# Kernel optimization log

Hardware: AMD Instinct MI355X
Metric: run time of the kernel (lower is better)

Reference implementation:

```python
import jax, jax.numpy as jnp
import numpy as np

E = 800_000      # number of edges
D = 256          # d_model_edge
N = 50_000       # number of atoms/nodes


def setup_inputs() -> dict:
    key = jax.random.key(0)
    k1, k2, k3, k4, k5 = jax.random.split(key, 5)
    forces = jax.random.normal(k1, (E, D), dtype=jnp.float32)
    V_st = jax.random.normal(k2, (E, 3), dtype=jnp.float32)
    # MLP([D, D, 1]): Linear(D,D) + act + Linear(D,1). Scaled init for stability.
    W1 = jax.random.normal(k3, (D, D), dtype=jnp.float32) * (1.0 / np.sqrt(D))
    b1 = jnp.zeros((D,), dtype=jnp.float32)
    W2 = jax.random.normal(k4, (D, 1), dtype=jnp.float32) * (1.0 / np.sqrt(D))
    b2 = jnp.zeros((1,), dtype=jnp.float32)
    idx_t = jax.random.randint(k5, (E,), 0, N, dtype=jnp.int64 if jax.config.jax_enable_x64 else jnp.int32)
    return {
        "forces": forces,
        "V_st": V_st,
        "W1": W1,
        "b1": b1,
        "W2": W2,
        "b2": b2,
        "idx_t": idx_t,
        "n_atoms": N,
    }


def reference(forces, V_st, W1, b1, W2, b2, idx_t, n_atoms):
    # out_mlp: Linear(D,D) -> SiLU -> Linear(D,1)
    h = jax.nn.silu(forces @ W1 + b1)          # [E, D]
    s = h @ W2 + b2                            # [E, 1] per-edge scalar
    ev = s * V_st                              # [E, 3] scaled direction vectors
    # scatter-sum over target node indices (reduction='sum')
    out = jax.ops.segment_sum(ev, idx_t, num_segments=n_atoms)  # [N, 3]
    return out
```

## Files before the change

kernel.cpp:

```cpp
#include <hip/hip_runtime.h>
#include <hip/hip_bf16.h>

typedef __attribute__((ext_vector_type(8))) short short8;
typedef __attribute__((ext_vector_type(4))) float floatx4;
typedef unsigned short u16;

#define D 256
#define BM 128
#define NT 512

__device__ __forceinline__ short f2bf(float f) {
    return __builtin_bit_cast(short, __float2bfloat16(f));
}

__global__ void w1f_kernel(const float* __restrict__ W1, u16* __restrict__ W1F) {
    const int k = blockIdx.x, n = threadIdx.x;
    const int k0t = k >> 5, g = (k >> 3) & 3, j = k & 7;
    const int nt = n >> 4, l15 = n & 15;
    W1F[(long)((((k0t << 4) + nt) << 6) + (g << 4) + l15) * 8 + j] = (u16)f2bf(W1[k * D + n]);
}

__launch_bounds__(NT, 4)
__global__ void head_kernel(const float* __restrict__ forces,
                            const float* __restrict__ V_st,
                            const u16*   __restrict__ W1F,
                            const float* __restrict__ b1,
                            const float* __restrict__ W2,
                            const float* __restrict__ b2,
                            const int*   __restrict__ idx_t,
                            float* __restrict__ out,
                            int E) {
    __shared__ u16 Abuf[BM * D];
    __shared__ float s_red[4][BM];

    const int tid  = threadIdx.x;
    const int lane = tid & 63;
    const int w    = tid >> 6;
    const int wm   = w >> 2;
    const int wn   = w & 3;
    const int l15  = lane & 15;
    const int g    = lane >> 4;

    const long blk_row = (long)blockIdx.x * BM;

#pragma unroll
    for (int it = 0; it < 8; ++it) {
        int c   = it * NT + tid;
        int row = c >> 5;
        int kc  = (c & 31) * 8;
        long grow = blk_row + row;
        if (grow > (long)E - 1) grow = (long)E - 1;
        const float* src = forces + grow * D + kc;
        floatx4 f0 = *(const floatx4*)(src);
        floatx4 f1 = *(const floatx4*)(src + 4);
        short8 a;
#pragma unroll
        for (int jj = 0; jj < 4; ++jj) { a[jj] = f2bf(f0[jj]); a[4 + jj] = f2bf(f1[jj]); }
        int off = (row * 512 + kc * 2) ^ ((row & 7) << 4);
        *(short8*)((char*)Abuf + off) = a;
    }
    __syncthreads();

    floatx4 acc[4][4];
#pragma unroll
    for (int mr = 0; mr < 4; ++mr)
#pragma unroll
        for (int nc = 0; nc < 4; ++nc)
            acc[mr][nc] = (floatx4){0.f, 0.f, 0.f, 0.f};

#pragma unroll
    for (int k0t = 0; k0t < 8; ++k0t) {
        short8 af[4], bfr[4];
#pragma unroll
        for (int mr = 0; mr < 4; ++mr) {
            int row = wm * 64 + mr * 16 + l15;
            int off = (row * 512 + k0t * 64 + g * 16) ^ ((row & 7) << 4);
            af[mr] = *(const short8*)((const char*)Abuf + off);
        }
#pragma unroll
        for (int nc = 0; nc < 4; ++nc) {
            int nt = wn * 4 + nc;
            bfr[nc] = *(const short8*)(W1F + (long)((k0t * 16 + nt) * 64 + lane) * 8);
        }
#pragma unroll
        for (int mr = 0; mr < 4; ++mr)
#pragma unroll
            for (int nc = 0; nc < 4; ++nc)
                acc[mr][nc] = __builtin_amdgcn_mfma_f32_16x16x32_bf16(
                    af[mr], bfr[nc], acc[mr][nc], 0, 0, 0);
    }

    float b1v[4], w2v[4];
#pragma unroll
    for (int nc = 0; nc < 4; ++nc) {
        int n = wn * 64 + nc * 16 + l15;
        b1v[nc] = b1[n];
        w2v[nc] = W2[n];
    }
    float part[4][4];
#pragma unroll
    for (int mr = 0; mr < 4; ++mr)
#pragma unroll
        for (int r = 0; r < 4; ++r) {
            float s = 0.f;
#pragma unroll
            for (int nc = 0; nc < 4; ++nc) {
                float z = acc[mr][nc][r] + b1v[nc];
                float h = z / (1.f + __expf(-z));
                s += h * w2v[nc];
            }
            part[mr][r] = s;
        }

#pragma unroll
    for (int off = 1; off < 16; off <<= 1)
#pragma unroll
        for (int mr = 0; mr < 4; ++mr)
#pragma unroll
            for (int r = 0; r < 4; ++r)
                part[mr][r] += __shfl_xor(part[mr][r], off, 16);

    if (l15 == 0) {
#pragma unroll
        for (int mr = 0; mr < 4; ++mr)
#pragma unroll
            for (int r = 0; r < 4; ++r)
                s_red[wn][wm * 64 + mr * 16 + g * 4 + r] = part[mr][r];
    }
    __syncthreads();

    if (tid < BM) {
        long e = blk_row + tid;
        if (e < E) {
            float s = s_red[0][tid] + s_red[1][tid] + s_red[2][tid] + s_red[3][tid] + b2[0];
            float vx = V_st[e * 3 + 0], vy = V_st[e * 3 + 1], vz = V_st[e * 3 + 2];
            long node = (long)idx_t[e];
            atomicAdd(&out[node * 3 + 0], s * vx);
            atomicAdd(&out[node * 3 + 1], s * vy);
            atomicAdd(&out[node * 3 + 2], s * vz);
        }
    }
}

extern "C" void kernel_launch(void* const* d_in, const int* in_sizes, int n_in,
                              void* d_out, int out_size, void* d_ws, size_t ws_size,
                              hipStream_t stream) {
    const float* forces = (const float*)d_in[0];
    const float* V_st   = (const float*)d_in[1];
    const float* W1     = (const float*)d_in[2];
    const float* b1     = (const float*)d_in[3];
    const float* W2     = (const float*)d_in[4];
    const float* b2     = (const float*)d_in[5];
    const int*   idx    = (const int*)d_in[6];
    const int E = in_sizes[6];

    u16* W1F = (u16*)d_ws;

    hipMemsetAsync(d_out, 0, (size_t)out_size * sizeof(float), stream);
    w1f_kernel<<<D, D, 0, stream>>>(W1, W1F);
    const int grid = (E + BM - 1) / BM;
    head_kernel<<<grid, NT, 0, stream>>>(forces, V_st, W1F, b1, W2, b2, idx,
                                         (float*)d_out, E);
}
```

Measured before the change: 298.7 us.

## Persistent head kernel with double-buffered async global-to-LDS loads

Turns the head kernel into a persistent grid of 1024 blocks that loop over edge tiles. Each tile is split into two K-halves, staged as fp32 into LDS with global_load_lds and double-buffered so the next load overlaps the MFMA compute, with bf16 conversion moved to LDS read time. It also folds the output memset and the W1 conversion into one prep kernel to cut launches. The cost is a larger fp32 LDS footprint, lower occupancy (launch bounds 2), extra syncs per tile, and a per-read conversion.

```diff
diff --git a/kernel.cpp b/kernel.cpp
--- a/kernel.cpp
+++ b/kernel.cpp
@@ -8,19 +8,32 @@
 #define D 256
 #define BM 128
 #define NT 512
+#define GRID 1024
 
 __device__ __forceinline__ short f2bf(float f) {
     return __builtin_bit_cast(short, __float2bfloat16(f));
 }
 
-__global__ void w1f_kernel(const float* __restrict__ W1, u16* __restrict__ W1F) {
-    const int k = blockIdx.x, n = threadIdx.x;
-    const int k0t = k >> 5, g = (k >> 3) & 3, j = k & 7;
-    const int nt = n >> 4, l15 = n & 15;
-    W1F[(long)((((k0t << 4) + nt) << 6) + (g << 4) + l15) * 8 + j] = (u16)f2bf(W1[k * D + n]);
-}
-
-__launch_bounds__(NT, 4)
+__global__ void prep_kernel(const float* __restrict__ W1, u16* __restrict__ W1F,
+                            float* __restrict__ out, int outn) {
+    const int b = blockIdx.x;
+    if (b < D) {
+        const int k = b, n = threadIdx.x;
+        const int k0t = k >> 5, g = (k >> 3) & 3, j = k & 7;
+        const int nt = n >> 4, l15 = n & 15;
+        W1F[(long)((((k0t << 4) + nt) << 6) + (g << 4) + l15) * 8 + j] = (u16)f2bf(W1[k * D + n]);
+    } else {
+        int i = (b - D) * 256 + threadIdx.x;
+        const int stride = (gridDim.x - D) * 256;
+        for (; i < outn; i += stride) out[i] = 0.f;
+    }
+}
+
+#define GLOAD_LDS(g, l) __builtin_amdgcn_global_load_lds( \
+    (const __attribute__((address_space(1))) unsigned int*)(g), \
+    (__attribute__((address_space(3))) unsigned int*)(l), 16, 0, 0)
+
+__launch_bounds__(NT, 2)
 __global__ void head_kernel(const float* __restrict__ forces,
                             const float* __restrict__ V_st,
                             const u16*   __restrict__ W1F,
@@ -30,7 +43,7 @@
                             const int*   __restrict__ idx_t,
                             float* __restrict__ out,
                             int E) {
-    __shared__ u16 Abuf[BM * D];
+    __shared__ float Abuf[2][BM * 128];
     __shared__ float s_red[4][BM];
 
     const int tid  = threadIdx.x;
@@ -40,26 +53,24 @@
     const int wn   = w & 3;
     const int l15  = lane & 15;
     const int g    = lane >> 4;
-
-    const long blk_row = (long)blockIdx.x * BM;
-
-#pragma unroll
-    for (int it = 0; it < 8; ++it) {
-        int c   = it * NT + tid;
-        int row = c >> 5;
-        int kc  = (c & 31) * 8;
-        long grow = blk_row + row;
-        if (grow > (long)E - 1) grow = (long)E - 1;
-        const float* src = forces + grow * D + kc;
-        floatx4 f0 = *(const floatx4*)(src);
-        floatx4 f1 = *(const floatx4*)(src + 4);
-        short8 a;
-#pragma unroll
-        for (int jj = 0; jj < 4; ++jj) { a[jj] = f2bf(f0[jj]); a[4 + jj] = f2bf(f1[jj]); }
-        int off = (row * 512 + kc * 2) ^ ((row & 7) << 4);
-        *(short8*)((char*)Abuf + off) = a;
-    }
-    __syncthreads();
+    const int q    = l15 & 7;
+
+    const int ntiles = (E + BM - 1) / BM;
+
+    const int ldsrow0 = w * 16;
+    const int lsub    = lane >> 5;
+    const int c31     = lane & 31;
+
+    auto STAGE = [&](int buf, long tile, int kh) {
+#pragma unroll
+        for (int j = 0; j < 8; ++j) {
+            long rowg = tile * BM + ldsrow0 + 2 * j + lsub;
+            if (rowg > (long)E - 1) rowg = (long)E - 1;
+            const float* src = forces + rowg * D + kh * 128
+                             + ((c31 ^ ((int)rowg & 7)) << 2);
+            GLOAD_LDS(src, &Abuf[buf][(ldsrow0 + 2 * j) * 128]);
+        }
+    };
 
     floatx4 acc[4][4];
 #pragma unroll
@@ -67,28 +78,6 @@
 #pragma unroll
         for (int nc = 0; nc < 4; ++nc)
             acc[mr][nc] = (floatx4){0.f, 0.f, 0.f, 0.f};
-
-#pragma unroll
-    for (int k0t = 0; k0t < 8; ++k0t) {
-        short8 af[4], bfr[4];
-#pragma unroll
-        for (int mr = 0; mr < 4; ++mr) {
-            int row = wm * 64 + mr * 16 + l15;
-            int off = (row * 512 + k0t * 64 + g * 16) ^ ((row & 7) << 4);
-            af[mr] = *(const short8*)((const char*)Abuf + off);
-        }
-#pragma unroll
-        for (int nc = 0; nc < 4; ++nc) {
-            int nt = wn * 4 + nc;
-            bfr[nc] = *(const short8*)(W1F + (long)((k0t * 16 + nt) * 64 + lane) * 8);
-        }
-#pragma unroll
-        for (int mr = 0; mr < 4; ++mr)
-#pragma unroll
-            for (int nc = 0; nc < 4; ++nc)
-                acc[mr][nc] = __builtin_amdgcn_mfma_f32_16x16x32_bf16(
-                    af[mr], bfr[nc], acc[mr][nc], 0, 0, 0);
-    }
 
     float b1v[4], w2v[4];
 #pragma unroll
@@ -97,48 +86,101 @@
         b1v[nc] = b1[n];
         w2v[nc] = W2[n];
     }
-    float part[4][4];
-#pragma unroll
-    for (int mr = 0; mr < 4; ++mr)
-#pragma unroll
-        for (int r = 0; r < 4; ++r) {
-            float s = 0.f;
+    const float b2v = b2[0];
+
+    auto COMPUTE = [&](int buf, int kh) {
+#pragma unroll
+        for (int kl = 0; kl < 4; ++kl) {
+            const int k0t = kh * 4 + kl;
+            short8 bfr[4];
 #pragma unroll
             for (int nc = 0; nc < 4; ++nc) {
-                float z = acc[mr][nc][r] + b1v[nc];
-                float h = z / (1.f + __expf(-z));
-                s += h * w2v[nc];
-            }
-            part[mr][r] = s;
-        }
-
-#pragma unroll
-    for (int off = 1; off < 16; off <<= 1)
+                int nt = wn * 4 + nc;
+                bfr[nc] = *(const short8*)(W1F + (long)((k0t * 16 + nt) * 64 + lane) * 8);
+            }
+            const int cg = kl * 8 + 2 * g;
+            short8 af[4];
+#pragma unroll
+            for (int mr = 0; mr < 4; ++mr) {
+                int row = wm * 64 + mr * 16 + l15;
+                floatx4 f0 = *(const floatx4*)&Abuf[buf][row * 128 + ((cg ^ q) << 2)];
+                floatx4 f1 = *(const floatx4*)&Abuf[buf][row * 128 + (((cg + 1) ^ q) << 2)];
+                short8 a;
+#pragma unroll
+                for (int jj = 0; jj < 4; ++jj) { a[jj] = f2bf(f0[jj]); a[4 + jj] = f2bf(f1[jj]); }
+                af[mr] = a;
+            }
+#pragma unroll
+            for (int mr = 0; mr < 4; ++mr)
+#pragma unroll
+                for (int nc = 0; nc < 4; ++nc)
+                    acc[mr][nc] = __builtin_amdgcn_mfma_f32_16x16x32_bf16(
+                        af[mr], bfr[nc], acc[mr][nc], 0, 0, 0);
+        }
+    };
+
+    long t = blockIdx.x;
+    if (t < (long)ntiles) STAGE(0, t, 0);
+    __syncthreads();
+
+    for (; t < (long)ntiles; ) {
+        STAGE(1, t, 1);
+        COMPUTE(0, 0);
+        __syncthreads();
+
+        const long tn = t + GRID;
+        if (tn < (long)ntiles) STAGE(0, tn, 0);
+        COMPUTE(1, 1);
+
+        float part[4][4];
 #pragma unroll
         for (int mr = 0; mr < 4; ++mr)
 #pragma unroll
-            for (int r = 0; r < 4; ++r)
-                part[mr][r] += __shfl_xor(part[mr][r], off, 16);
-
-    if (l15 == 0) {
+            for (int r = 0; r < 4; ++r) {
+                float s = 0.f;
+#pragma unroll
+                for (int nc = 0; nc < 4; ++nc) {
+                    float z = acc[mr][nc][r] + b1v[nc];
+                    float h = z / (1.f + __expf(-z));
+                    s += h * w2v[nc];
+                }
+                part[mr][r] = s;
+            }
 #pragma unroll
         for (int mr = 0; mr < 4; ++mr)
 #pragma unroll
-            for (int r = 0; r < 4; ++r)
-                s_red[wn][wm * 64 + mr * 16 + g * 4 + r] = part[mr][r];
-    }
-    __syncthreads();
-
-    if (tid < BM) {
-        long e = blk_row + tid;
-        if (e < E) {
-            float s = s_red[0][tid] + s_red[1][tid] + s_red[2][tid] + s_red[3][tid] + b2[0];
-            float vx = V_st[e * 3 + 0], vy = V_st[e * 3 + 1], vz = V_st[e * 3 + 2];
-            long node = (long)idx_t[e];
-            atomicAdd(&out[node * 3 + 0], s * vx);
-            atomicAdd(&out[node * 3 + 1], s * vy);
-            atomicAdd(&out[node * 3 + 2], s * vz);
-        }
+            for (int nc = 0; nc < 4; ++nc)
+                acc[mr][nc] = (floatx4){0.f, 0.f, 0.f, 0.f};
+
+#pragma unroll
+        for (int off = 1; off < 16; off <<= 1)
+#pragma unroll
+            for (int mr = 0; mr < 4; ++mr)
+#pragma unroll
+                for (int r = 0; r < 4; ++r)
+                    part[mr][r] += __shfl_xor(part[mr][r], off, 16);
+
+        if (l15 == 0) {
+#pragma unroll
+            for (int mr = 0; mr < 4; ++mr)
+#pragma unroll
+                for (int r = 0; r < 4; ++r)
+                    s_red[wn][wm * 64 + mr * 16 + g * 4 + r] = part[mr][r];
+        }
+        __syncthreads();
+
+        if (tid < BM) {
+            long e = t * BM + tid;
+            if (e < E) {
+                float s = s_red[0][tid] + s_red[1][tid] + s_red[2][tid] + s_red[3][tid] + b2v;
+                float vx = V_st[e * 3 + 0], vy = V_st[e * 3 + 1], vz = V_st[e * 3 + 2];
+                long node = (long)idx_t[e];
+                atomicAdd(&out[node * 3 + 0], s * vx);
+                atomicAdd(&out[node * 3 + 1], s * vy);
+                atomicAdd(&out[node * 3 + 2], s * vz);
+            }
+        }
+        t = tn;
     }
 }
 
@@ -156,9 +198,7 @@
 
     u16* W1F = (u16*)d_ws;
 
-    hipMemsetAsync(d_out, 0, (size_t)out_size * sizeof(float), stream);
-    w1f_kernel<<<D, D, 0, stream>>>(W1, W1F);
-    const int grid = (E + BM - 1) / BM;
-    head_kernel<<<grid, NT, 0, stream>>>(forces, V_st, W1F, b1, W2, b2, idx,
+    prep_kernel<<<D + 128, 256, 0, stream>>>(W1, W1F, (float*)d_out, out_size);
+    head_kernel<<<GRID, NT, 0, stream>>>(forces, V_st, W1F, b1, W2, b2, idx,
                                          (float*)d_out, E);
 }
```

After: 377.1 us. 26.2% more time.
